# Performance work log

Hardware: AMD Instinct MI355X
Metric: run time of the kernel (lower is better)

The kernel has to match this reference:

```python
import jax, jax.numpy as jnp
import numpy as np

HEADS = 16
DIM_HEAD = 64
SCALE = DIM_HEAD ** -0.5


def setup_inputs() -> dict:
    key = jax.random.key(0)
    ks = jax.random.split(key, 6)
    B, Nq, Nkv, D = 2, 512, 4096, 1024
    inner = HEADS * DIM_HEAD  # 1024
    s = 1.0 / np.sqrt(D)
    return {
        "q": jax.random.normal(ks[0], (B, Nq, D), jnp.float32),
        "kv": jax.random.normal(ks[1], (B, Nkv, D), jnp.float32),
        "mask": jnp.ones((B, Nkv), dtype=bool),
        "Wq": jax.random.normal(ks[2], (D, inner), jnp.float32) * s,
        "Wkv": jax.random.normal(ks[3], (D, 2 * inner), jnp.float32) * s,
        "Wo": jax.random.normal(ks[4], (inner, D), jnp.float32) * (1.0 / np.sqrt(inner)),
        "bo": jnp.zeros((D,), jnp.float32),
    }


def reference(q, kv, mask, Wq, Wkv, Wo, bo):
    B, Nq, D = q.shape
    Nkv = kv.shape[1]
    h, dh = HEADS, DIM_HEAD
    # projections
    qh = (q @ Wq).reshape(B, Nq, h, dh).transpose(0, 2, 1, 3)        # (B,h,Nq,dh)
    kvp = kv @ Wkv                                                    # (B,Nkv,2*inner)
    k, v = jnp.split(kvp, 2, axis=-1)
    kh = k.reshape(B, Nkv, h, dh).transpose(0, 2, 1, 3)              # (B,h,Nkv,dh)
    vh = v.reshape(B, Nkv, h, dh).transpose(0, 2, 1, 3)
    # scaled dot-product cross-attention
    attn = jnp.einsum("bhqd,bhkd->bhqk", qh, kh) * SCALE             # (B,h,Nq,Nkv)
    neg_inf = jnp.finfo(attn.dtype).min
    attn = jnp.where(mask[:, None, None, :], attn, neg_inf)
    attn = jax.nn.softmax(attn, axis=-1)
    out = jnp.einsum("bhqk,bhkd->bhqd", attn, vh)                    # (B,h,Nq,dh)
    out = out.transpose(0, 2, 1, 3).reshape(B, Nq, h * dh)
    return out @ Wo + bo
```

## Files before the change

kernel.cpp:

```cpp
#include <hip/hip_runtime.h>
#include <string.h>
#include <math.h>

typedef unsigned short u16;
typedef __bf16 bf16x8 __attribute__((ext_vector_type(8)));
typedef float floatx4 __attribute__((ext_vector_type(4)));

#define HEADS  16
#define DH     64
#define BATCH  2
#define NQ     512
#define NKV    4096
#define DMODEL 1024
#define INNER  1024
#define SCALE  0.125f
#define LOG2E  1.4426950408889634f
#define SPLIT  4
#define KEYS_PER_PART (NKV / SPLIT)
#define CH (KEYS_PER_PART / 64)

__device__ __forceinline__ u16 f2bf(float f) {
  union { float f; unsigned int u; } v; v.f = f;
  unsigned int u = v.u;
  unsigned int r = u + 0x7fffu + ((u >> 16) & 1u);
  return (u16)(r >> 16);
}

__device__ __forceinline__ void gll16(const u16* g, u16* l) {
  __builtin_amdgcn_global_load_lds(
      (const __attribute__((address_space(1))) unsigned int*)g,
      (__attribute__((address_space(3))) unsigned int*)l, 16, 0, 0);
}

__global__ __launch_bounds__(256) void prep(const float* __restrict__ q,
                                            const float* __restrict__ kv,
                                            const float* __restrict__ Wq,
                                            const float* __restrict__ Wkv,
                                            const float* __restrict__ Wo,
                                            u16* __restrict__ qb,
                                            u16* __restrict__ kvb,
                                            u16* __restrict__ Wqt,
                                            u16* __restrict__ Wkvt,
                                            u16* __restrict__ Wot) {
  __shared__ float tile[32][33];
  const int bx = blockIdx.x, tid = threadIdx.x;
  if (bx < 4608) {
    const float* x; u16* y; size_t i;
    if (bx < 512) { x = q;  y = qb;  i = (size_t)bx * 256 + tid; }
    else          { x = kv; y = kvb; i = (size_t)(bx - 512) * 256 + tid; }
    const float4* p = (const float4*)x + i * 2;
    float4 a = p[0], b = p[1];
    union { u16 s[8]; uint4 v; } o;
    o.s[0] = f2bf(a.x); o.s[1] = f2bf(a.y); o.s[2] = f2bf(a.z); o.s[3] = f2bf(a.w);
    o.s[4] = f2bf(b.x); o.s[5] = f2bf(b.y); o.s[6] = f2bf(b.z); o.s[7] = f2bf(b.w);
    *(uint4*)(y + i * 8) = o.v;
    return;
  }
  const float* W; u16* Wt; int K, N, n0, k0, t;
  if (bx < 5632)      { t = bx - 4608; W = Wq;  Wt = Wqt;  K = 1024; N = 1024; n0 = (t & 31) * 32; k0 = (t >> 5) * 32; }
  else if (bx < 7680) { t = bx - 5632; W = Wkv; Wt = Wkvt; K = 1024; N = 2048; n0 = (t & 63) * 32; k0 = (t >> 6) * 32; }
  else                { t = bx - 7680; W = Wo;  Wt = Wot;  K = 1024; N = 1024; n0 = (t & 31) * 32; k0 = (t >> 5) * 32; }
  const int tx = tid & 31, ty = tid >> 5;
  for (int i = 0; i < 32; i += 8)
    tile[ty + i][tx] = W[(size_t)(k0 + ty + i) * N + n0 + tx];
  __syncthreads();
  for (int i = 0; i < 32; i += 8)
    Wt[(size_t)(n0 + ty + i) * K + k0 + tx] = f2bf(tile[tx][ty + i]);
}

__global__ __launch_bounds__(256) void gemm_kv(const u16* __restrict__ A,
                                               const u16* __restrict__ Bt,
                                               u16* __restrict__ Kb,
                                               u16* __restrict__ Vb) {
  const int K = DMODEL;
  __shared__ __align__(16) u16 As[128 * 32];
  __shared__ __align__(16) u16 Bs[128 * 32];
  const int tid  = threadIdx.x;
  const int lane = tid & 63, wave = tid >> 6;
  const int wr = wave >> 1, wc = wave & 1;
  const int l16 = lane & 15, quad = lane >> 4;
  const int bm = blockIdx.y, bn = blockIdx.x;
  const int r0 = tid >> 2;
  const int kb = (tid & 3) ^ ((tid >> 3) & 3);
  const u16* aP0 = A  + ((size_t)bm * 128 + r0)      * K + kb * 8;
  const u16* aP1 = A  + ((size_t)bm * 128 + r0 + 64) * K + kb * 8;
  const u16* bP0 = Bt + ((size_t)bn * 128 + r0)      * K + kb * 8;
  const u16* bP1 = Bt + ((size_t)bn * 128 + r0 + 64) * K + kb * 8;
  u16* ldsA0 = As + wave * 512;
  u16* ldsA1 = As + 2048 + wave * 512;
  u16* ldsB0 = Bs + wave * 512;
  u16* ldsB1 = Bs + 2048 + wave * 512;
  const int ko = ((quad ^ ((l16 >> 1) & 3)) << 3);

  floatx4 acc[4][4] = {};
  for (int k0 = 0; k0 < K; k0 += 32) {
    gll16(aP0 + k0, ldsA0);
    gll16(aP1 + k0, ldsA1);
    gll16(bP0 + k0, ldsB0);
    gll16(bP1 + k0, ldsB1);
    __syncthreads();
    bf16x8 af[4], bfr[4];
#pragma unroll
    for (int i = 0; i < 4; ++i)
      af[i] = *(const bf16x8*)&As[(wr * 64 + i * 16 + l16) * 32 + ko];
#pragma unroll
    for (int j = 0; j < 4; ++j)
      bfr[j] = *(const bf16x8*)&Bs[(wc * 64 + j * 16 + l16) * 32 + ko];
#pragma unroll
    for (int i = 0; i < 4; ++i)
#pragma unroll
      for (int j = 0; j < 4; ++j)
        acc[i][j] = __builtin_amdgcn_mfma_f32_16x16x32_bf16(af[i], bfr[j], acc[i][j], 0, 0, 0);
    __syncthreads();
  }
  u16* Cb = (bn < 8) ? Kb : Vb;
  const int colbase = ((bn < 8) ? bn : bn - 8) * 128;
#pragma unroll
  for (int i = 0; i < 4; ++i) {
    const int rowb = bm * 128 + wr * 64 + i * 16 + quad * 4;
#pragma unroll
    for (int j = 0; j < 4; ++j) {
      const int col = colbase + wc * 64 + j * 16 + l16;
#pragma unroll
      for (int r = 0; r < 4; ++r)
        Cb[(size_t)(rowb + r) * 1024 + col] = f2bf(acc[i][j][r]);
    }
  }
}

template<bool OUT_BF16>
__global__ __launch_bounds__(256) void gemm64(const u16* __restrict__ A,
                                              const u16* __restrict__ Bt,
                                              float* __restrict__ Cf,
                                              u16* __restrict__ Cb,
                                              const float* __restrict__ bias,
                                              int M, int N, int K) {
  __shared__ __align__(16) u16 As[64 * 64];
  __shared__ __align__(16) u16 Bs[64 * 64];
  const int tid = threadIdx.x;
  const int lane = tid & 63, wave = tid >> 6;
  const int wr = wave >> 1, wc = wave & 1;
  const int l16 = lane & 15, quad = lane >> 4;
  const int bm = blockIdx.y, bn = blockIdx.x;
  const int r0 = tid >> 3;
  const int kbs = (tid & 7) ^ (r0 & 7);
  const u16* aP0 = A  + ((size_t)bm * 64 + r0)      * K + kbs * 8;
  const u16* aP1 = A  + ((size_t)bm * 64 + r0 + 32) * K + kbs * 8;
  const u16* bP0 = Bt + ((size_t)bn * 64 + r0)      * K + kbs * 8;
  const u16* bP1 = Bt + ((size_t)bn * 64 + r0 + 32) * K + kbs * 8;
  u16* ldsA0 = As + wave * 512;
  u16* ldsA1 = As + 2048 + wave * 512;
  u16* ldsB0 = Bs + wave * 512;
  u16* ldsB1 = Bs + 2048 + wave * 512;

  floatx4 acc[2][2] = {};
  for (int k0 = 0; k0 < K; k0 += 64) {
    gll16(aP0 + k0, ldsA0);
    gll16(aP1 + k0, ldsA1);
    gll16(bP0 + k0, ldsB0);
    gll16(bP1 + k0, ldsB1);
    __syncthreads();
    bf16x8 af[2][2], bfr[2][2];
#pragma unroll
    for (int i = 0; i < 2; ++i)
#pragma unroll
      for (int kk = 0; kk < 2; ++kk)
        af[i][kk] = *(const bf16x8*)&As[(wr * 32 + i * 16 + l16) * 64 +
                                        (((kk * 4 + quad) ^ (l16 & 7)) << 3)];
#pragma unroll
    for (int j = 0; j < 2; ++j)
#pragma unroll
      for (int kk = 0; kk < 2; ++kk)
        bfr[j][kk] = *(const bf16x8*)&Bs[(wc * 32 + j * 16 + l16) * 64 +
                                         (((kk * 4 + quad) ^ (l16 & 7)) << 3)];
#pragma unroll
    for (int i = 0; i < 2; ++i)
#pragma unroll
      for (int j = 0; j < 2; ++j) {
        acc[i][j] = __builtin_amdgcn_mfma_f32_16x16x32_bf16(af[i][0], bfr[j][0], acc[i][j], 0, 0, 0);
        acc[i][j] = __builtin_amdgcn_mfma_f32_16x16x32_bf16(af[i][1], bfr[j][1], acc[i][j], 0, 0, 0);
      }
    __syncthreads();
  }
#pragma unroll
  for (int i = 0; i < 2; ++i) {
    const int rowb = bm * 64 + wr * 32 + i * 16 + quad * 4;
#pragma unroll
    for (int j = 0; j < 2; ++j) {
      const int col = bn * 64 + wc * 32 + j * 16 + l16;
#pragma unroll
      for (int r = 0; r < 4; ++r) {
        const size_t idx = (size_t)(rowb + r) * N + col;
        if (OUT_BF16) Cb[idx] = f2bf(acc[i][j][r]);
        else          Cf[idx] = acc[i][j][r] + bias[col];
      }
    }
  }
}

__global__ __launch_bounds__(256) void vtrans(const u16* __restrict__ Vb,
                                              u16* __restrict__ vT) {
  __shared__ u16 t[64 * 72];
  const int bx = blockIdx.x, tid = threadIdx.x;
  const int bh = bx >> 6, tb = bx & 63;
  const int b = bh >> 4, h = bh & 15;
  const int r = tid >> 2, cg = (tid & 3) * 16;
  const u16* src = Vb + ((size_t)(b * NKV + tb * 64 + r)) * 1024 + h * 64 + cg;
  *(uint4*)&t[r * 72 + cg]     = ((const uint4*)src)[0];
  *(uint4*)&t[r * 72 + cg + 8] = ((const uint4*)src)[1];
  __syncthreads();
  const int d = tid >> 2, tg = (tid & 3) * 16;
  union { u16 s[16]; uint4 v[2]; } o;
#pragma unroll
  for (int i = 0; i < 16; ++i) o.s[i] = t[(tg + i) * 72 + d];
  u16* dst = vT + ((size_t)(bh * 64 + d)) * NKV + tb * 64 + tg;
  *(uint4*)dst = o.v[0]; *(uint4*)(dst + 8) = o.v[1];
}

__global__ __launch_bounds__(256) void attn_part(const u16* __restrict__ Qh,
                                                 const u16* __restrict__ Kb,
                                                 const u16* __restrict__ vT,
                                                 const int* __restrict__ mask,
                                                 float* __restrict__ Opart,
                                                 float* __restrict__ Mst,
                                                 float* __restrict__ Lst) {
  __shared__ __align__(16) u16 Qs[64 * 72];
  __shared__ __align__(16) u16 Ks[64 * 64];
  __shared__ __align__(16) u16 Vs[64 * 64];
  __shared__ __align__(16) u16 Ps[4][16 * 72];
  __shared__ float Msk[64];
  const int tid = threadIdx.x;
  const int lane = tid & 63, w = tid >> 6;
  const int l16 = lane & 15, quad = lane >> 4;
  const int part = blockIdx.x & (SPLIT - 1);
  const int qt = (blockIdx.x >> 2) & 7;
  const int h  = (blockIdx.x >> 5) & 15;
  const int b  = blockIdx.x >> 9;
  const int rs = tid >> 2, d0 = (tid & 3) * 16;

  {
    const uint4* p = (const uint4*)(Qh + ((size_t)(b * NQ + qt * 64 + rs)) * INNER + h * DH + d0);
    *(uint4*)&Qs[rs * 72 + d0]     = p[0];
    *(uint4*)&Qs[rs * 72 + d0 + 8] = p[1];
  }
  __syncthreads();
  bf16x8 aq0 = *(const bf16x8*)&Qs[(w * 16 + l16) * 72 + quad * 8];
  bf16x8 aq1 = *(const bf16x8*)&Qs[(w * 16 + l16) * 72 + 32 + quad * 8];

  const int r8 = lane >> 3;
  const int kb8 = (lane & 7) ^ (r8 & 7);
  const int key00 = part * KEYS_PER_PART;
  const u16* kSrc = Kb + ((size_t)(b * NKV + key00 + w * 8 + r8)) * 1024 + h * DH + kb8 * 8;
  const u16* vSrc = vT + ((size_t)((b * 16 + h) * 64 + w * 8 + r8)) * NKV + key00 + kb8 * 8;
  u16* ldsK0 = Ks + w * 512;
  u16* ldsK1 = Ks + 2048 + w * 512;
  u16* ldsV0 = Vs + w * 512;
  u16* ldsV1 = Vs + 2048 + w * 512;
  const int koA = (quad ^ (l16 & 7)) << 3;
  const int koB = ((quad + 4) ^ (l16 & 7)) << 3;

  floatx4 o[4] = {};
  float m_r[4] = {-1e30f, -1e30f, -1e30f, -1e30f};
  float l_r[4] = {0.f, 0.f, 0.f, 0.f};

  for (int c = 0; c < CH; ++c) {
    const int key0 = key00 + c * 64;
    gll16(kSrc + (size_t)c * 65536, ldsK0);
    gll16(kSrc + (size_t)c * 65536 + 32768, ldsK1);
    gll16(vSrc + c * 64, ldsV0);
    gll16(vSrc + c * 64 + (size_t)32 * NKV, ldsV1);
    if (tid < 64) Msk[tid] = (mask[(size_t)b * NKV + key0 + tid] != 0) ? 0.0f : -1e30f;
    __syncthreads();

    float sv[4][4];
#pragma unroll
    for (int nt = 0; nt < 4; ++nt) {
      bf16x8 b0 = *(const bf16x8*)&Ks[(nt * 16 + l16) * 64 + koA];
      bf16x8 b1 = *(const bf16x8*)&Ks[(nt * 16 + l16) * 64 + koB];
      floatx4 t = {0.f, 0.f, 0.f, 0.f};
      t = __builtin_amdgcn_mfma_f32_16x16x32_bf16(aq0, b0, t, 0, 0, 0);
      t = __builtin_amdgcn_mfma_f32_16x16x32_bf16(aq1, b1, t, 0, 0, 0);
      const float mk = Msk[nt * 16 + l16];
#pragma unroll
      for (int r = 0; r < 4; ++r) sv[nt][r] = t[r] * (SCALE * LOG2E) + mk;
    }
    float mnew[4], alpha[4], psum[4];
#pragma unroll
    for (int r = 0; r < 4; ++r) {
      float t = fmaxf(fmaxf(sv[0][r], sv[1][r]), fmaxf(sv[2][r], sv[3][r]));
      t = fmaxf(t, __shfl_xor(t, 1));
      t = fmaxf(t, __shfl_xor(t, 2));
      t = fmaxf(t, __shfl_xor(t, 4));
      t = fmaxf(t, __shfl_xor(t, 8));
      mnew[r] = fmaxf(m_r[r], t);
      alpha[r] = exp2f(m_r[r] - mnew[r]);
      m_r[r] = mnew[r];
      psum[r] = 0.f;
    }
#pragma unroll
    for (int nt = 0; nt < 4; ++nt)
#pragma unroll
      for (int r = 0; r < 4; ++r) {
        float p = exp2f(sv[nt][r] - mnew[r]);
        psum[r] += p;
        Ps[w][(quad * 4 + r) * 72 + nt * 16 + l16] = f2bf(p);
      }
#pragma unroll
    for (int r = 0; r < 4; ++r) {
      float t = psum[r];
      t += __shfl_xor(t, 1);
      t += __shfl_xor(t, 2);
      t += __shfl_xor(t, 4);
      t += __shfl_xor(t, 8);
      l_r[r] = l_r[r] * alpha[r] + t;
#pragma unroll
      for (int dt = 0; dt < 4; ++dt) o[dt][r] *= alpha[r];
    }
    bf16x8 ap0 = *(const bf16x8*)&Ps[w][l16 * 72 + quad * 8];
    bf16x8 ap1 = *(const bf16x8*)&Ps[w][l16 * 72 + 32 + quad * 8];
#pragma unroll
    for (int dt = 0; dt < 4; ++dt) {
      bf16x8 bv0 = *(const bf16x8*)&Vs[(dt * 16 + l16) * 64 + koA];
      bf16x8 bv1 = *(const bf16x8*)&Vs[(dt * 16 + l16) * 64 + koB];
      o[dt] = __builtin_amdgcn_mfma_f32_16x16x32_bf16(ap0, bv0, o[dt], 0, 0, 0);
      o[dt] = __builtin_amdgcn_mfma_f32_16x16x32_bf16(ap1, bv1, o[dt], 0, 0, 0);
    }
    __syncthreads();
  }
  const int pid = blockIdx.x;
#pragma unroll
  for (int r = 0; r < 4; ++r) {
    const int q = w * 16 + quad * 4 + r;
    if (l16 == 0) { Mst[pid * 64 + q] = m_r[r]; Lst[pid * 64 + q] = l_r[r]; }
#pragma unroll
    for (int dt = 0; dt < 4; ++dt)
      Opart[(size_t)pid * 4096 + q * 64 + dt * 16 + l16] = o[dt][r];
  }
}

__global__ __launch_bounds__(256) void attn_combine(const float* __restrict__ Opart,
                                                    const float* __restrict__ Mst,
                                                    const float* __restrict__ Lst,
                                                    u16* __restrict__ Out) {
  const int x = blockIdx.x;
  const int t = threadIdx.x;
  const int q = t >> 2, db = (t & 3) * 16;
  const int b = x >> 7, h = (x >> 3) & 15, qt = x & 7;
  float ms[SPLIT], ls[SPLIT];
#pragma unroll
  for (int s = 0; s < SPLIT; ++s) {
    ms[s] = Mst[(size_t)(x * SPLIT + s) * 64 + q];
    ls[s] = Lst[(size_t)(x * SPLIT + s) * 64 + q];
  }
  float M = fmaxf(fmaxf(ms[0], ms[1]), fmaxf(ms[2], ms[3]));
  float wgt[SPLIT], L = 0.f;
#pragma unroll
  for (int s = 0; s < SPLIT; ++s) { wgt[s] = exp2f(ms[s] - M); L += wgt[s] * ls[s]; }
  const float inv = 1.0f / L;
  float acc[16] = {};
#pragma unroll
  for (int s = 0; s < SPLIT; ++s) {
    const float4* p = (const float4*)&Opart[(size_t)(x * SPLIT + s) * 4096 + q * 64 + db];
    const float ws = wgt[s];
#pragma unroll
    for (int i = 0; i < 4; ++i) {
      float4 v = p[i];
      acc[i * 4 + 0] += ws * v.x; acc[i * 4 + 1] += ws * v.y;
      acc[i * 4 + 2] += ws * v.z; acc[i * 4 + 3] += ws * v.w;
    }
  }
  union { u16 s[16]; uint4 v[2]; } ou;
#pragma unroll
  for (int i = 0; i < 16; ++i) ou.s[i] = f2bf(acc[i] * inv);
  u16* dst = Out + ((size_t)(b * NQ + qt * 64 + q)) * INNER + h * DH + db;
  *(uint4*)dst = ou.v[0]; *(uint4*)(dst + 8) = ou.v[1];
}

extern "C" void kernel_launch(void* const* d_in, const int* in_sizes, int n_in,
                              void* d_out, int out_size, void* d_ws, size_t ws_size,
                              hipStream_t stream) {
  const float* q    = (const float*)d_in[0];
  const float* kv   = (const float*)d_in[1];
  const int*   mask = (const int*)d_in[2];
  const float* Wq   = (const float*)d_in[3];
  const float* Wkv  = (const float*)d_in[4];
  const float* Wo   = (const float*)d_in[5];
  const float* bo   = (const float*)d_in[6];
  float* out = (float*)d_out;

  char* ws = (char*)d_ws;
  u16*   qb    = (u16*)(ws);
  u16*   kvb   = (u16*)(ws + (2u << 20));
  float* Mst   = (float*)(ws);
  float* Lst   = (float*)(ws + (256u << 10));
  u16*   vT    = (u16*)(ws + (2u << 20));
  u16* Wqt  = (u16*)(ws + (18u << 20));
  u16* Wkvt = (u16*)(ws + (20u << 20));
  u16* Wot  = (u16*)(ws + (24u << 20));
  u16* qh   = (u16*)(ws + (26u << 20));
  u16* Kb   = (u16*)(ws + (28u << 20));
  u16* Vb   = (u16*)(ws + (44u << 20));
  float* Opart = (float*)(ws + (44u << 20));
  u16* attn = (u16*)(ws + (60u << 20));

  prep<<<dim3(8704), 256, 0, stream>>>(q, kv, Wq, Wkv, Wo, qb, kvb, Wqt, Wkvt, Wot);
  gemm64<true><<<dim3(INNER / 64, (BATCH * NQ) / 64), 256, 0, stream>>>(
      qb, Wqt, nullptr, qh, nullptr, BATCH * NQ, INNER, DMODEL);
  gemm_kv<<<dim3(16, 64), 256, 0, stream>>>(kvb, Wkvt, Kb, Vb);
  vtrans<<<dim3(BATCH * HEADS * (NKV / 64)), 256, 0, stream>>>(Vb, vT);
  attn_part<<<dim3(BATCH * HEADS * (NQ / 64) * SPLIT), 256, 0, stream>>>(
      qh, Kb, vT, mask, Opart, Mst, Lst);
  attn_combine<<<dim3(BATCH * HEADS * (NQ / 64)), 256, 0, stream>>>(Opart, Mst, Lst, attn);
  gemm64<false><<<dim3(DMODEL / 64, (BATCH * NQ) / 64), 256, 0, stream>>>(
      attn, Wot, out, nullptr, bo, BATCH * NQ, DMODEL, INNER);
}
```

Baseline: 247.8 us.

## Prefetch next K/V chunk during PV matmul with double-buffered V

Restructures the attention loop so the next chunk's K, V and mask loads are issued after the QK/softmax phase and overlap with the P·V MFMAs. V is double-buffered, and the Q staging buffer is reused as the P scratch to save LDS. f2bf is also replaced with the native __bf16 conversion. This adds a second barrier per iteration and relies on async global-to-LDS loads completing before the next barrier.

```diff
diff --git a/kernel.cpp b/kernel.cpp
--- a/kernel.cpp
+++ b/kernel.cpp
@@ -20,10 +20,7 @@
 #define CH (KEYS_PER_PART / 64)
 
 __device__ __forceinline__ u16 f2bf(float f) {
-  union { float f; unsigned int u; } v; v.f = f;
-  unsigned int u = v.u;
-  unsigned int r = u + 0x7fffu + ((u >> 16) & 1u);
-  return (u16)(r >> 16);
+  union { __bf16 h; u16 u; } v; v.h = (__bf16)f; return v.u;
 }
 
 __device__ __forceinline__ void gll16(const u16* g, u16* l) {
@@ -224,10 +221,9 @@
                                                  float* __restrict__ Opart,
                                                  float* __restrict__ Mst,
                                                  float* __restrict__ Lst) {
-  __shared__ __align__(16) u16 Qs[64 * 72];
   __shared__ __align__(16) u16 Ks[64 * 64];
-  __shared__ __align__(16) u16 Vs[64 * 64];
-  __shared__ __align__(16) u16 Ps[4][16 * 72];
+  __shared__ __align__(16) u16 Vs[2][64 * 64];
+  __shared__ __align__(16) u16 QP[4608];
   __shared__ float Msk[64];
   const int tid = threadIdx.x;
   const int lane = tid & 63, w = tid >> 6;
@@ -237,15 +233,7 @@
   const int h  = (blockIdx.x >> 5) & 15;
   const int b  = blockIdx.x >> 9;
   const int rs = tid >> 2, d0 = (tid & 3) * 16;
-
-  {
-    const uint4* p = (const uint4*)(Qh + ((size_t)(b * NQ + qt * 64 + rs)) * INNER + h * DH + d0);
-    *(uint4*)&Qs[rs * 72 + d0]     = p[0];
-    *(uint4*)&Qs[rs * 72 + d0 + 8] = p[1];
-  }
-  __syncthreads();
-  bf16x8 aq0 = *(const bf16x8*)&Qs[(w * 16 + l16) * 72 + quad * 8];
-  bf16x8 aq1 = *(const bf16x8*)&Qs[(w * 16 + l16) * 72 + 32 + quad * 8];
+  u16* Ps = QP + w * 1152;
 
   const int r8 = lane >> 3;
   const int kb8 = (lane & 7) ^ (r8 & 7);
@@ -254,24 +242,32 @@
   const u16* vSrc = vT + ((size_t)((b * 16 + h) * 64 + w * 8 + r8)) * NKV + key00 + kb8 * 8;
   u16* ldsK0 = Ks + w * 512;
   u16* ldsK1 = Ks + 2048 + w * 512;
-  u16* ldsV0 = Vs + w * 512;
-  u16* ldsV1 = Vs + 2048 + w * 512;
   const int koA = (quad ^ (l16 & 7)) << 3;
   const int koB = ((quad + 4) ^ (l16 & 7)) << 3;
+
+  {
+    const uint4* p = (const uint4*)(Qh + ((size_t)(b * NQ + qt * 64 + rs)) * INNER + h * DH + d0);
+    *(uint4*)&QP[rs * 72 + d0]     = p[0];
+    *(uint4*)&QP[rs * 72 + d0 + 8] = p[1];
+  }
+  gll16(kSrc, ldsK0);
+  gll16(kSrc + 32768, ldsK1);
+  gll16(vSrc, Vs[0] + w * 512);
+  gll16(vSrc + (size_t)32 * NKV, Vs[0] + 2048 + w * 512);
+  float mk0 = 0.f;
+  if (tid < 64) mk0 = (mask[(size_t)b * NKV + key00 + tid] != 0) ? 0.0f : -1e30f;
+  __syncthreads();
+  bf16x8 aq0 = *(const bf16x8*)&QP[(w * 16 + l16) * 72 + quad * 8];
+  bf16x8 aq1 = *(const bf16x8*)&QP[(w * 16 + l16) * 72 + 32 + quad * 8];
+  if (tid < 64) Msk[tid] = mk0;
+  __syncthreads();
 
   floatx4 o[4] = {};
   float m_r[4] = {-1e30f, -1e30f, -1e30f, -1e30f};
   float l_r[4] = {0.f, 0.f, 0.f, 0.f};
 
   for (int c = 0; c < CH; ++c) {
-    const int key0 = key00 + c * 64;
-    gll16(kSrc + (size_t)c * 65536, ldsK0);
-    gll16(kSrc + (size_t)c * 65536 + 32768, ldsK1);
-    gll16(vSrc + c * 64, ldsV0);
-    gll16(vSrc + c * 64 + (size_t)32 * NKV, ldsV1);
-    if (tid < 64) Msk[tid] = (mask[(size_t)b * NKV + key0 + tid] != 0) ? 0.0f : -1e30f;
-    __syncthreads();
-
+    const u16* Vcur = Vs[c & 1];
     float sv[4][4];
 #pragma unroll
     for (int nt = 0; nt < 4; ++nt) {
@@ -303,7 +299,7 @@
       for (int r = 0; r < 4; ++r) {
         float p = exp2f(sv[nt][r] - mnew[r]);
         psum[r] += p;
-        Ps[w][(quad * 4 + r) * 72 + nt * 16 + l16] = f2bf(p);
+        Ps[(quad * 4 + r) * 72 + nt * 16 + l16] = f2bf(p);
       }
 #pragma unroll
     for (int r = 0; r < 4; ++r) {
@@ -316,12 +312,22 @@
 #pragma unroll
       for (int dt = 0; dt < 4; ++dt) o[dt][r] *= alpha[r];
     }
-    bf16x8 ap0 = *(const bf16x8*)&Ps[w][l16 * 72 + quad * 8];
-    bf16x8 ap1 = *(const bf16x8*)&Ps[w][l16 * 72 + 32 + quad * 8];
+    __syncthreads();
+    if (c + 1 < CH) {
+      gll16(kSrc + (size_t)(c + 1) * 65536, ldsK0);
+      gll16(kSrc + (size_t)(c + 1) * 65536 + 32768, ldsK1);
+      u16* vdst = Vs[(c + 1) & 1];
+      gll16(vSrc + (c + 1) * 64, vdst + w * 512);
+      gll16(vSrc + (c + 1) * 64 + (size_t)32 * NKV, vdst + 2048 + w * 512);
+      if (tid < 64)
+        Msk[tid] = (mask[(size_t)b * NKV + key00 + (c + 1) * 64 + tid] != 0) ? 0.0f : -1e30f;
+    }
+    bf16x8 ap0 = *(const bf16x8*)&Ps[l16 * 72 + quad * 8];
+    bf16x8 ap1 = *(const bf16x8*)&Ps[l16 * 72 + 32 + quad * 8];
 #pragma unroll
     for (int dt = 0; dt < 4; ++dt) {
-      bf16x8 bv0 = *(const bf16x8*)&Vs[(dt * 16 + l16) * 64 + koA];
-      bf16x8 bv1 = *(const bf16x8*)&Vs[(dt * 16 + l16) * 64 + koB];
+      bf16x8 bv0 = *(const bf16x8*)&Vcur[(dt * 16 + l16) * 64 + koA];
+      bf16x8 bv1 = *(const bf16x8*)&Vcur[(dt * 16 + l16) * 64 + koB];
       o[dt] = __builtin_amdgcn_mfma_f32_16x16x32_bf16(ap0, bv0, o[dt], 0, 0, 0);
       o[dt] = __builtin_amdgcn_mfma_f32_16x16x32_bf16(ap1, bv1, o[dt], 0, 0, 0);
     }
```

New measurement: 247.7 us. Within noise of the previous version (-0.0%).
